# Kernel tuning notes

Measured on AMD Instinct MI355X. Metric: run time of the kernel, lower is better.

## Reference

```python
import jax, jax.numpy as jnp
import numpy as np

D_MODEL = 2048
N_HEADS = 16
D_K = D_MODEL // N_HEADS
NB_FEAT = 8  # ceil(ln(2048))
BLOCK_H = 1
BLOCK_W = 1
EPS = 1e-6


def setup_inputs() -> dict:
    key = jax.random.key(0)
    ks = jax.random.split(key, 8)
    B, S = 2, 4096
    q = jax.random.normal(ks[0], (B, S, D_MODEL), dtype=jnp.float32)
    k = jax.random.normal(ks[1], (B, S, D_MODEL), dtype=jnp.float32)
    v = jax.random.normal(ks[2], (B, S, D_MODEL), dtype=jnp.float32)
    # torch Linear weights [out, in]
    w_q = jax.random.normal(ks[3], (D_MODEL, D_MODEL), dtype=jnp.float32) / np.sqrt(D_MODEL)
    w_k = jax.random.normal(ks[4], (D_MODEL, D_MODEL), dtype=jnp.float32) / np.sqrt(D_MODEL)
    w_v = jax.random.normal(ks[5], (D_MODEL, D_MODEL), dtype=jnp.float32) / np.sqrt(D_MODEL)
    w_o = jax.random.normal(ks[6], (D_MODEL, D_MODEL), dtype=jnp.float32) / np.sqrt(D_MODEL)
    omega = jax.random.normal(ks[7], (NB_FEAT, D_K), dtype=jnp.float32) / np.sqrt(D_K)
    return {"q": q, "k": k, "v": v, "w_q": w_q, "w_k": w_k, "w_v": w_v, "w_o": w_o, "omega": omega}


def _kernel(x):
    # kernel_type == 'exp'
    return jnp.exp(-0.5 * x * x)


def reference(q, k, v, w_q, w_k, w_v, w_o, omega):
    B, Sq, D = q.shape
    Sk = k.shape[1]
    # projections (torch Linear: x @ W.T), split heads -> [B, S, H, d_k]
    qh = (q @ w_q.T).reshape(B, Sq, N_HEADS, D_K)
    kh = (k @ w_k.T).reshape(B, Sk, N_HEADS, D_K)
    vh = (v @ w_v.T).reshape(B, Sk, N_HEADS, D_K)
    # random-feature maps -> [B, S, H, nb]
    q_prime = _kernel(jnp.einsum('bshd,nd->bshn', qh, omega))
    k_prime = _kernel(jnp.einsum('bshd,nd->bshn', kh, omega))
    q_prime = q_prime / (q_prime.sum(-1, keepdims=True) + EPS)
    k_prime = k_prime / (k_prime.sum(-1, keepdims=True) + EPS)
    # causal prefix sums along sequence
    K_cum = jnp.cumsum(k_prime, axis=1)                                   # [B,S,H,nb]
    KV_cum = jnp.cumsum(k_prime[..., None] * vh[..., None, :], axis=1)    # [B,S,H,nb,d_k]
    # blockwise causal key selection
    q_idx = jnp.arange(Sq)
    key_idx = jnp.minimum((q_idx // BLOCK_H + 1) * BLOCK_W - 1, Sk - 1)   # [Sq]
    K_sel = K_cum[:, key_idx]    # [B,Sq,H,nb]
    KV_sel = KV_cum[:, key_idx]  # [B,Sq,H,nb,d_k]
    numerator = jnp.einsum('bshn,bshnd->bshd', q_prime, KV_sel)
    denominator = jnp.sum(q_prime * K_sel, axis=-1, keepdims=True)
    out = numerator / (denominator + EPS)
    out = out.reshape(B, Sq, D)
    return out @ w_o.T
```

## Files before the change

### kernel.cpp

```cpp
#include <hip/hip_runtime.h>
#include <hip/hip_bf16.h>
#include <cstdint>

#define B_SZ 2
#define S_LEN 4096
#define R_TOT 8192
#define DM 2048
#define NH 16
#define DK 128
#define NFEAT 8
#define CHUNK 128
#define NCHUNK 32
#define KSPL 512
#define EPSF 1e-6f

typedef short bf16x8_t __attribute__((ext_vector_type(8)));
typedef float f32x4_t __attribute__((ext_vector_type(4)));

__device__ __forceinline__ ushort f2bf(float f) {
  uint32_t u = __float_as_uint(f);
  u += 0x7FFF + ((u >> 16) & 1);
  return (ushort)(u >> 16);
}
__device__ __forceinline__ float bf2f(ushort u) {
  return __uint_as_float(((uint32_t)u) << 16);
}

__global__ __launch_bounds__(256) void cast_f32_bf16(const float* __restrict__ src,
                                                     ushort* __restrict__ dst, int n4) {
  int i = blockIdx.x * 256 + threadIdx.x;
  if (i >= n4) return;
  float4 f = reinterpret_cast<const float4*>(src)[i];
  ushort4 o;
  o.x = f2bf(f.x); o.y = f2bf(f.y); o.z = f2bf(f.z); o.w = f2bf(f.w);
  reinterpret_cast<ushort4*>(dst)[i] = o;
}

__global__ __launch_bounds__(256) void fold_kernel(const float* __restrict__ W,
                                                   const float* __restrict__ omega,
                                                   ushort* __restrict__ O) {
  __shared__ float som[NFEAT * DK];
  const int h = blockIdx.y;
  const int j = blockIdx.x * 256 + threadIdx.x;
  for (int i = threadIdx.x; i < NFEAT * DK; i += 256) som[i] = omega[i];
  __syncthreads();
  float acc[NFEAT] = {0.f, 0.f, 0.f, 0.f, 0.f, 0.f, 0.f, 0.f};
  for (int d = 0; d < DK; d++) {
    const float w = W[(size_t)(h * DK + d) * DM + j];
#pragma unroll
    for (int n = 0; n < NFEAT; n++) acc[n] += w * som[n * DK + d];
  }
#pragma unroll
  for (int n = 0; n < NFEAT; n++) O[(size_t)(h * NFEAT + n) * DM + j] = f2bf(acc[n]);
}

template<int BF16OUT>
__global__ __launch_bounds__(512, 1) void gemm256(const ushort* __restrict__ A,
                                                  const ushort* __restrict__ Bm,
                                                  void* __restrict__ Cv,
                                                  int M, int N, int K) {
  __shared__ ushort lds[8 * 8192];
  const int tid = threadIdx.x;
  const int wave = tid >> 6, lane = tid & 63;
  const int wm = wave >> 2, wn = wave & 3;
  const int NKT = K >> 6;

  const int nb = N >> 8;
  const int cpx = gridDim.x >> 3;
  const int swz = (blockIdx.x & 7) * cpx + (blockIdx.x >> 3);
  const int bx = swz % nb, by = swz / nb;
  const int m0 = by * 256, n0 = bx * 256;

  auto stage = [&](int bufi, int ab, int kh, int kt, const ushort* G, int r0) {
    ushort* Lr = lds + (((bufi << 1) | ab) << 1 | kh) * 8192;
#pragma unroll
    for (int j = 0; j < 2; j++) {
      const int c = j * 512 + wave * 64 + lane;
      const int row = c >> 2, slot = c & 3;
      const int ss = slot ^ ((row >> 1) & 3);
      const ushort* g = G + (size_t)(r0 + row) * K + kt * 64 + kh * 32 + ss * 8;
      __builtin_amdgcn_global_load_lds(
          (const __attribute__((address_space(1))) void*)g,
          (__attribute__((address_space(3))) void*)(Lr + (j * 512 + wave * 64) * 8), 16, 0, 0);
    }
  };
  auto rdA = [&](int bufi, int kh, int m) -> bf16x8_t {
    const int row = wm * 128 + m * 16 + (lane & 15);
    const int slot = (lane >> 4) ^ ((row >> 1) & 3);
    return *reinterpret_cast<const bf16x8_t*>(lds + ((bufi << 2) | kh) * 8192 + row * 32 + slot * 8);
  };
  auto rdB = [&](int bufi, int kh, int nf) -> bf16x8_t {
    const int row = wn * 64 + nf * 16 + (lane & 15);
    const int slot = (lane >> 4) ^ ((row >> 1) & 3);
    return *reinterpret_cast<const bf16x8_t*>(lds + (((bufi << 1) | 1) << 1 | kh) * 8192 + row * 32 + slot * 8);
  };

  f32x4_t acc[8][4];
#pragma unroll
  for (int m = 0; m < 8; m++)
#pragma unroll
    for (int nf = 0; nf < 4; nf++) acc[m][nf] = (f32x4_t){0.f, 0.f, 0.f, 0.f};

  stage(0, 0, 0, 0, A, m0);  stage(0, 1, 0, 0, Bm, n0);
  stage(0, 0, 1, 0, A, m0);  stage(0, 1, 1, 0, Bm, n0);
  stage(1, 0, 0, 1, A, m0);  stage(1, 1, 0, 1, Bm, n0);
  asm volatile("s_waitcnt vmcnt(4)" ::: "memory");
  __builtin_amdgcn_s_barrier();
  __builtin_amdgcn_sched_barrier(0);

  bf16x8_t afr[8], b0, b1;
  for (int t = 0; t < NKT; t++) {
    const int buf = t & 1;
#pragma unroll
    for (int m = 0; m < 8; m++) afr[m] = rdA(buf, 0, m);
    b0 = rdB(buf, 0, 0); b1 = rdB(buf, 0, 1);
    if (t + 1 < NKT) { stage(buf ^ 1, 0, 1, t + 1, A, m0); stage(buf ^ 1, 1, 1, t + 1, Bm, n0); }
    __builtin_amdgcn_s_barrier();
    __builtin_amdgcn_s_setprio(1);
#pragma unroll
    for (int m = 0; m < 8; m++) {
      acc[m][0] = __builtin_amdgcn_mfma_f32_16x16x32_bf16(afr[m], b0, acc[m][0], 0, 0, 0);
      acc[m][1] = __builtin_amdgcn_mfma_f32_16x16x32_bf16(afr[m], b1, acc[m][1], 0, 0, 0);
    }
    __builtin_amdgcn_s_setprio(0);
    __builtin_amdgcn_s_barrier();
    __builtin_amdgcn_sched_barrier(0);
    b0 = rdB(buf, 0, 2); b1 = rdB(buf, 0, 3);
    __builtin_amdgcn_s_barrier();
    __builtin_amdgcn_s_setprio(1);
#pragma unroll
    for (int m = 0; m < 8; m++) {
      acc[m][2] = __builtin_amdgcn_mfma_f32_16x16x32_bf16(afr[m], b0, acc[m][2], 0, 0, 0);
      acc[m][3] = __builtin_amdgcn_mfma_f32_16x16x32_bf16(afr[m], b1, acc[m][3], 0, 0, 0);
    }
    __builtin_amdgcn_s_setprio(0);
    __builtin_amdgcn_s_barrier();
    __builtin_amdgcn_sched_barrier(0);
#pragma unroll
    for (int m = 0; m < 8; m++) afr[m] = rdA(buf, 1, m);
    b0 = rdB(buf, 1, 0); b1 = rdB(buf, 1, 1);
    if (t + 2 < NKT) { stage(buf, 0, 0, t + 2, A, m0); stage(buf, 1, 0, t + 2, Bm, n0); }
    __builtin_amdgcn_s_barrier();
    __builtin_amdgcn_s_setprio(1);
#pragma unroll
    for (int m = 0; m < 8; m++) {
      acc[m][0] = __builtin_amdgcn_mfma_f32_16x16x32_bf16(afr[m], b0, acc[m][0], 0, 0, 0);
      acc[m][1] = __builtin_amdgcn_mfma_f32_16x16x32_bf16(afr[m], b1, acc[m][1], 0, 0, 0);
    }
    __builtin_amdgcn_s_setprio(0);
    __builtin_amdgcn_s_barrier();
    __builtin_amdgcn_sched_barrier(0);
    b0 = rdB(buf, 1, 2); b1 = rdB(buf, 1, 3);
    __builtin_amdgcn_s_barrier();
    __builtin_amdgcn_s_setprio(1);
#pragma unroll
    for (int m = 0; m < 8; m++) {
      acc[m][2] = __builtin_amdgcn_mfma_f32_16x16x32_bf16(afr[m], b0, acc[m][2], 0, 0, 0);
      acc[m][3] = __builtin_amdgcn_mfma_f32_16x16x32_bf16(afr[m], b1, acc[m][3], 0, 0, 0);
    }
    __builtin_amdgcn_s_setprio(0);
    if (t + 2 < NKT) { asm volatile("s_waitcnt vmcnt(4)" ::: "memory"); }
    else             { asm volatile("s_waitcnt vmcnt(0)" ::: "memory"); }
    __builtin_amdgcn_s_barrier();
    __builtin_amdgcn_sched_barrier(0);
  }

#pragma unroll
  for (int m = 0; m < 8; m++) {
    const int rb = m0 + wm * 128 + m * 16 + (lane >> 4) * 4;
#pragma unroll
    for (int nf = 0; nf < 4; nf++) {
      const int col = n0 + wn * 64 + nf * 16 + (lane & 15);
#pragma unroll
      for (int r = 0; r < 4; r++) {
        const float val = acc[m][nf][r];
        if (BF16OUT)
          ((ushort*)Cv)[(size_t)(rb + r) * N + col] = f2bf(val);
        else
          ((float*)Cv)[(size_t)(rb + r) * N + col] = val;
      }
    }
  }
}

__global__ __launch_bounds__(256) void gemm_thin(const ushort* __restrict__ A,
                                                 const ushort* __restrict__ Bm,
                                                 float* __restrict__ P,
                                                 int M, int K) {
  __shared__ ushort lds_a[128 * 32];
  __shared__ ushort lds_b[128 * 32];
  const int t = threadIdx.x;
  const int wave = t >> 6, lane = t & 63;
  const int spl = blockIdx.x;
  const int m0 = blockIdx.y * 128;
  const int kb = spl * KSPL;
  const int wm = wave >> 1, wn = wave & 1;

  f32x4_t acc[4][4];
#pragma unroll
  for (int i = 0; i < 4; i++)
#pragma unroll
    for (int j = 0; j < 4; j++) acc[i][j] = (f32x4_t){0.f, 0.f, 0.f, 0.f};

  const int srow = lane >> 2;
  const int skoff = (lane & 3) * 8;

  for (int k0 = kb; k0 < kb + KSPL; k0 += 32) {
#pragma unroll
    for (int i = 0; i < 2; i++) {
      const int rgrp = i * 4 + wave;
      const int row = rgrp * 16 + srow;
      const ushort* ga = A + (size_t)(m0 + row) * K + (k0 + skoff);
      const ushort* gb = Bm + (size_t)row * K + (k0 + skoff);
      __builtin_amdgcn_global_load_lds(
          (const __attribute__((address_space(1))) void*)ga,
          (__attribute__((address_space(3))) void*)(lds_a + rgrp * 512), 16, 0, 0);
      __builtin_amdgcn_global_load_lds(
          (const __attribute__((address_space(1))) void*)gb,
          (__attribute__((address_space(3))) void*)(lds_b + rgrp * 512), 16, 0, 0);
    }
    __syncthreads();
    bf16x8_t af[4], bfr[4];
#pragma unroll
    for (int i = 0; i < 4; i++) {
      af[i]  = *reinterpret_cast<const bf16x8_t*>(
          lds_a + (wm * 64 + i * 16 + (lane & 15)) * 32 + (lane >> 4) * 8);
      bfr[i] = *reinterpret_cast<const bf16x8_t*>(
          lds_b + (wn * 64 + i * 16 + (lane & 15)) * 32 + (lane >> 4) * 8);
    }
#pragma unroll
    for (int i = 0; i < 4; i++)
#pragma unroll
      for (int j = 0; j < 4; j++)
        acc[i][j] = __builtin_amdgcn_mfma_f32_16x16x32_bf16(af[i], bfr[j], acc[i][j], 0, 0, 0);
    __syncthreads();
  }

  float* Pp = P + (size_t)spl * ((size_t)R_TOT * 128);
#pragma unroll
  for (int i = 0; i < 4; i++) {
    const int rb = m0 + wm * 64 + i * 16 + (lane >> 4) * 4;
#pragma unroll
    for (int j = 0; j < 4; j++) {
      const int col = wn * 64 + j * 16 + (lane & 15);
#pragma unroll
      for (int r = 0; r < 4; r++)
        Pp[(size_t)(rb + r) * 128 + col] = acc[i][j][r];
    }
  }
}

__global__ __launch_bounds__(256) void feat2_kernel(const float* __restrict__ P,
                                                    float* __restrict__ F) {
  const int g = blockIdx.x * 256 + threadIdx.x;
  const int row = g >> 4, h = g & 15;
  float4 a = {0.f, 0.f, 0.f, 0.f}, c = {0.f, 0.f, 0.f, 0.f};
#pragma unroll
  for (int s = 0; s < 4; s++) {
    const float4* xp = reinterpret_cast<const float4*>(
        P + (size_t)s * ((size_t)R_TOT * 128) + (size_t)row * 128 + h * NFEAT);
    const float4 u = xp[0], w = xp[1];
    a.x += u.x; a.y += u.y; a.z += u.z; a.w += u.w;
    c.x += w.x; c.y += w.y; c.z += w.z; c.w += w.w;
  }
  float x[8] = {a.x, a.y, a.z, a.w, c.x, c.y, c.z, c.w};
  float f[8], s = 0.f;
#pragma unroll
  for (int n = 0; n < 8; n++) { f[n] = __expf(-0.5f * x[n] * x[n]); s += f[n]; }
  const float inv = 1.f / (s + EPSF);
  const int b = row >> 12, sidx = row & 4095;
  float* out = F + ((size_t)(h * 2 + b) * 4096 + sidx) * 8;
  float4 o0 = {f[0] * inv, f[1] * inv, f[2] * inv, f[3] * inv};
  float4 o1 = {f[4] * inv, f[5] * inv, f[6] * inv, f[7] * inv};
  reinterpret_cast<float4*>(out)[0] = o0;
  reinterpret_cast<float4*>(out)[1] = o1;
}

__global__ __launch_bounds__(128) void chunk_sum_kernel(const float* __restrict__ KF,
                                                        const ushort* __restrict__ VH,
                                                        float* __restrict__ CKV,
                                                        float* __restrict__ CK) {
  const int cid = blockIdx.x;
  const int c = cid & 31, bh = cid >> 5, b = bh >> 4, h = bh & 15;
  const int d = threadIdx.x;
  __shared__ float s_kf[CHUNK * 8];
  const size_t fbase = ((size_t)(h * 2 + b) * 4096 + (size_t)c * CHUNK) * 8;
  {
    float4 a0 = *reinterpret_cast<const float4*>(KF + fbase + d * 8);
    float4 a1 = *reinterpret_cast<const float4*>(KF + fbase + d * 8 + 4);
    *reinterpret_cast<float4*>(s_kf + d * 8) = a0;
    *reinterpret_cast<float4*>(s_kf + d * 8 + 4) = a1;
  }
  __syncthreads();
  float kv[8] = {0, 0, 0, 0, 0, 0, 0, 0};
  float ks = 0.f;
  const ushort* vp = VH + ((size_t)b * S_LEN + (size_t)c * CHUNK) * DM + h * DK + d;
  for (int s = 0; s < CHUNK; s++) {
    const float v = bf2f(vp[(size_t)s * DM]);
#pragma unroll
    for (int n = 0; n < 8; n++) kv[n] += s_kf[s * 8 + n] * v;
    ks += s_kf[s * 8 + (d & 7)];
  }
#pragma unroll
  for (int n = 0; n < 8; n++) CKV[((size_t)cid * 8 + n) * 128 + d] = kv[n];
  if (d < 8) CK[cid * 8 + d] = ks;
}

__global__ __launch_bounds__(128) void chunk_scan2(float* __restrict__ CKV,
                                                   float* __restrict__ CK) {
  const int bh = blockIdx.x >> 3, n = blockIdx.x & 7;
  const int d = threadIdx.x;
  float v[NCHUNK];
#pragma unroll
  for (int c = 0; c < NCHUNK; c++)
    v[c] = CKV[((size_t)(bh * NCHUNK + c) * 8 + n) * 128 + d];
  float run = 0.f;
#pragma unroll
  for (int c = 0; c < NCHUNK; c++) {
    const float tv = v[c];
    CKV[((size_t)(bh * NCHUNK + c) * 8 + n) * 128 + d] = run;
    run += tv;
  }
  if (d < 32) {
    const int i = (bh * NCHUNK + d) * 8 + n;
    const float orig = CK[i];
    float inc = orig;
#pragma unroll
    for (int off = 1; off < 32; off <<= 1) {
      const float o = __shfl_up(inc, off, 32);
      if (d >= off) inc += o;
    }
    CK[i] = inc - orig;
  }
}

__global__ __launch_bounds__(128) void attn_scan_kernel(const float* __restrict__ QF,
                                                        const float* __restrict__ KF,
                                                        const ushort* __restrict__ VH,
                                                        const float* __restrict__ CKV,
                                                        const float* __restrict__ CK,
                                                        ushort* __restrict__ AO) {
  const int cid = blockIdx.x;
  const int c = cid & 31, bh = cid >> 5, b = bh >> 4, h = bh & 15;
  const int d = threadIdx.x;
  __shared__ float s_qf[CHUNK * 8];
  __shared__ float s_kf[CHUNK * 8];
  const size_t fbase = ((size_t)(h * 2 + b) * 4096 + (size_t)c * CHUNK) * 8;
  {
    float4 a0 = *reinterpret_cast<const float4*>(QF + fbase + d * 8);
    float4 a1 = *reinterpret_cast<const float4*>(QF + fbase + d * 8 + 4);
    float4 b0 = *reinterpret_cast<const float4*>(KF + fbase + d * 8);
    float4 b1 = *reinterpret_cast<const float4*>(KF + fbase + d * 8 + 4);
    *reinterpret_cast<float4*>(s_qf + d * 8) = a0;
    *reinterpret_cast<float4*>(s_qf + d * 8 + 4) = a1;
    *reinterpret_cast<float4*>(s_kf + d * 8) = b0;
    *reinterpret_cast<float4*>(s_kf + d * 8 + 4) = b1;
  }
  float kv[8], krun[8];
#pragma unroll
  for (int n = 0; n < 8; n++) kv[n] = CKV[((size_t)cid * 8 + n) * 128 + d];
#pragma unroll
  for (int n = 0; n < 8; n++) krun[n] = CK[cid * 8 + n];
  __syncthreads();
  const size_t row0 = (size_t)b * S_LEN + (size_t)c * CHUNK;
  const ushort* vp = VH + row0 * DM + h * DK + d;
  ushort* op = AO + row0 * DM + h * DK + d;
  for (int s = 0; s < CHUNK; s++) {
    const float v = bf2f(vp[(size_t)s * DM]);
    float num = 0.f, den = 0.f;
#pragma unroll
    for (int n = 0; n < 8; n++) {
      const float kf = s_kf[s * 8 + n];
      kv[n] += kf * v;
      krun[n] += kf;
      const float qf = s_qf[s * 8 + n];
      num += qf * kv[n];
      den += qf * krun[n];
    }
    op[(size_t)s * DM] = f2bf(num / (den + EPSF));
  }
}

extern "C" void kernel_launch(void* const* d_in, const int* in_sizes, int n_in,
                              void* d_out, int out_size, void* d_ws, size_t ws_size,
                              hipStream_t stream) {
  const float* q     = (const float*)d_in[0];
  const float* k     = (const float*)d_in[1];
  const float* v     = (const float*)d_in[2];
  const float* w_q   = (const float*)d_in[3];
  const float* w_k   = (const float*)d_in[4];
  const float* w_v   = (const float*)d_in[5];
  const float* w_o   = (const float*)d_in[6];
  const float* omega = (const float*)d_in[7];

  char* ws = (char*)d_ws;
  const size_t DD2 = (size_t)DM * DM * 2;
  const size_t OD2 = (size_t)NH * NFEAT * DM * 2;
  const size_t RD2 = (size_t)R_TOT * DM * 2;
  const size_t X4  = (size_t)R_TOT * NH * NFEAT * 4;

  ushort* wvb = (ushort*)(ws);
  ushort* wob = (ushort*)(ws + DD2);
  ushort* oqb = (ushort*)(ws + 2 * DD2);
  ushort* okb = (ushort*)(ws + 2 * DD2 + OD2);
  ushort* xb  = (ushort*)(ws + 2 * DD2 + 2 * OD2);
  ushort* vhb = (ushort*)(ws + 2 * DD2 + 2 * OD2 + RD2);
  float*  xp4 = (float*) (ws + 2 * DD2 + 2 * OD2 + RD2);
  float*  qf  = (float*) (ws + 2 * DD2 + 2 * OD2 + 2 * RD2);
  float*  kf  = (float*) (ws + 2 * DD2 + 2 * OD2 + 2 * RD2 + X4);
  float*  ckv = (float*) (ws + 2 * DD2 + 2 * OD2 + 2 * RD2 + 2 * X4);
  float*  ck  = (float*) (ws + 2 * DD2 + 2 * OD2 + 2 * RD2 + 3 * X4);
  ushort* ao  = xb;

  const int n4_in = R_TOT * DM / 4;
  const int n4_w  = DM * DM / 4;

  cast_f32_bf16<<<dim3(n4_w / 256), 256, 0, stream>>>(w_v, wvb, n4_w);
  cast_f32_bf16<<<dim3(n4_w / 256), 256, 0, stream>>>(w_o, wob, n4_w);
  fold_kernel<<<dim3(DM / 256, NH), 256, 0, stream>>>(w_q, omega, oqb);
  fold_kernel<<<dim3(DM / 256, NH), 256, 0, stream>>>(w_k, omega, okb);

  dim3 gg_thin(DM / KSPL, R_TOT / 128);

  cast_f32_bf16<<<dim3(n4_in / 256), 256, 0, stream>>>(q, xb, n4_in);
  gemm_thin<<<gg_thin, 256, 0, stream>>>(xb, oqb, xp4, R_TOT, DM);
  feat2_kernel<<<dim3(R_TOT * NH / 256), 256, 0, stream>>>(xp4, qf);

  cast_f32_bf16<<<dim3(n4_in / 256), 256, 0, stream>>>(k, xb, n4_in);
  gemm_thin<<<gg_thin, 256, 0, stream>>>(xb, okb, xp4, R_TOT, DM);
  feat2_kernel<<<dim3(R_TOT * NH / 256), 256, 0, stream>>>(xp4, kf);

  cast_f32_bf16<<<dim3(n4_in / 256), 256, 0, stream>>>(v, xb, n4_in);
  gemm256<1><<<dim3((R_TOT / 256) * (DM / 256)), 512, 0, stream>>>(xb, wvb, (void*)vhb, R_TOT, DM, DM);

  chunk_sum_kernel<<<dim3(B_SZ * NH * NCHUNK), 128, 0, stream>>>(kf, vhb, ckv, ck);
  chunk_scan2<<<dim3(B_SZ * NH * 8), 128, 0, stream>>>(ckv, ck);
  attn_scan_kernel<<<dim3(B_SZ * NH * NCHUNK), 128, 0, stream>>>(qf, kf, vhb, ckv, ck, ao);

  gemm256<0><<<dim3((R_TOT / 256) * (DM / 256)), 512, 0, stream>>>(ao, wob, d_out, R_TOT, DM, DM);
}
```

Before: 349.2 us.

## Reschedule GEMM main loop into quarter-tile MFMA clusters with interleaved staging

Restructures the bf16 MFMA GEMM inner loop. Each half-k step is now split into two clusters of 16 MFMAs: four A fragments by four B fragments. The A and B global-to-LDS stages are issued separately between clusters, and explicit lgkmcnt waits are placed before each cluster. Boundary iterations now always issue loads by clamping the tile index (redundant loads at the tail) rather than branching, and vmcnt waits become a uniform count. The aim is to spread global loads more evenly and cut register pressure from holding 8 A fragments. The cost is extra redundant loads at the end and more barriers per iteration.

Measured after the change: 350.3 us. Within noise of the previous version (+0.3%).

```diff
diff --git a/kernel.cpp b/kernel.cpp
--- a/kernel.cpp
+++ b/kernel.cpp
@@ -104,66 +104,125 @@
   stage(0, 0, 0, 0, A, m0);  stage(0, 1, 0, 0, Bm, n0);
   stage(0, 0, 1, 0, A, m0);  stage(0, 1, 1, 0, Bm, n0);
   stage(1, 0, 0, 1, A, m0);  stage(1, 1, 0, 1, Bm, n0);
-  asm volatile("s_waitcnt vmcnt(4)" ::: "memory");
+  asm volatile("s_waitcnt vmcnt(8)" ::: "memory");
   __builtin_amdgcn_s_barrier();
   __builtin_amdgcn_sched_barrier(0);
 
-  bf16x8_t afr[8], b0, b1;
+  bf16x8_t a0, a1, a2, a3, b0, b1, b2, b3;
   for (int t = 0; t < NKT; t++) {
     const int buf = t & 1;
-#pragma unroll
-    for (int m = 0; m < 8; m++) afr[m] = rdA(buf, 0, m);
-    b0 = rdB(buf, 0, 0); b1 = rdB(buf, 0, 1);
-    if (t + 1 < NKT) { stage(buf ^ 1, 0, 1, t + 1, A, m0); stage(buf ^ 1, 1, 1, t + 1, Bm, n0); }
-    __builtin_amdgcn_s_barrier();
+    const int t1 = (t + 1 < NKT) ? t + 1 : NKT - 1;
+    const int t2 = (t + 2 < NKT) ? t + 2 : NKT - 1;
+
+    a0 = rdA(buf, 0, 0); a1 = rdA(buf, 0, 1); a2 = rdA(buf, 0, 2); a3 = rdA(buf, 0, 3);
+    b0 = rdB(buf, 0, 0); b1 = rdB(buf, 0, 1); b2 = rdB(buf, 0, 2); b3 = rdB(buf, 0, 3);
+    stage(buf ^ 1, 0, 1, t1, A, m0);
+    __builtin_amdgcn_s_barrier();
+    asm volatile("s_waitcnt lgkmcnt(0)" ::: "memory");
+    __builtin_amdgcn_sched_barrier(0);
     __builtin_amdgcn_s_setprio(1);
-#pragma unroll
-    for (int m = 0; m < 8; m++) {
-      acc[m][0] = __builtin_amdgcn_mfma_f32_16x16x32_bf16(afr[m], b0, acc[m][0], 0, 0, 0);
-      acc[m][1] = __builtin_amdgcn_mfma_f32_16x16x32_bf16(afr[m], b1, acc[m][1], 0, 0, 0);
-    }
+    acc[0][0] = __builtin_amdgcn_mfma_f32_16x16x32_bf16(a0, b0, acc[0][0], 0, 0, 0);
+    acc[1][0] = __builtin_amdgcn_mfma_f32_16x16x32_bf16(a1, b0, acc[1][0], 0, 0, 0);
+    acc[2][0] = __builtin_amdgcn_mfma_f32_16x16x32_bf16(a2, b0, acc[2][0], 0, 0, 0);
+    acc[3][0] = __builtin_amdgcn_mfma_f32_16x16x32_bf16(a3, b0, acc[3][0], 0, 0, 0);
+    acc[0][1] = __builtin_amdgcn_mfma_f32_16x16x32_bf16(a0, b1, acc[0][1], 0, 0, 0);
+    acc[1][1] = __builtin_amdgcn_mfma_f32_16x16x32_bf16(a1, b1, acc[1][1], 0, 0, 0);
+    acc[2][1] = __builtin_amdgcn_mfma_f32_16x16x32_bf16(a2, b1, acc[2][1], 0, 0, 0);
+    acc[3][1] = __builtin_amdgcn_mfma_f32_16x16x32_bf16(a3, b1, acc[3][1], 0, 0, 0);
+    acc[0][2] = __builtin_amdgcn_mfma_f32_16x16x32_bf16(a0, b2, acc[0][2], 0, 0, 0);
+    acc[1][2] = __builtin_amdgcn_mfma_f32_16x16x32_bf16(a1, b2, acc[1][2], 0, 0, 0);
+    acc[2][2] = __builtin_amdgcn_mfma_f32_16x16x32_bf16(a2, b2, acc[2][2], 0, 0, 0);
+    acc[3][2] = __builtin_amdgcn_mfma_f32_16x16x32_bf16(a3, b2, acc[3][2], 0, 0, 0);
+    acc[0][3] = __builtin_amdgcn_mfma_f32_16x16x32_bf16(a0, b3, acc[0][3], 0, 0, 0);
+    acc[1][3] = __builtin_amdgcn_mfma_f32_16x16x32_bf16(a1, b3, acc[1][3], 0, 0, 0);
+    acc[2][3] = __builtin_amdgcn_mfma_f32_16x16x32_bf16(a2, b3, acc[2][3], 0, 0, 0);
+    acc[3][3] = __builtin_amdgcn_mfma_f32_16x16x32_bf16(a3, b3, acc[3][3], 0, 0, 0);
     __builtin_amdgcn_s_setprio(0);
     __builtin_amdgcn_s_barrier();
     __builtin_amdgcn_sched_barrier(0);
-    b0 = rdB(buf, 0, 2); b1 = rdB(buf, 0, 3);
-    __builtin_amdgcn_s_barrier();
+
+    a0 = rdA(buf, 0, 4); a1 = rdA(buf, 0, 5); a2 = rdA(buf, 0, 6); a3 = rdA(buf, 0, 7);
+    stage(buf ^ 1, 1, 1, t1, Bm, n0);
+    __builtin_amdgcn_s_barrier();
+    asm volatile("s_waitcnt lgkmcnt(0)" ::: "memory");
+    __builtin_amdgcn_sched_barrier(0);
     __builtin_amdgcn_s_setprio(1);
-#pragma unroll
-    for (int m = 0; m < 8; m++) {
-      acc[m][2] = __builtin_amdgcn_mfma_f32_16x16x32_bf16(afr[m], b0, acc[m][2], 0, 0, 0);
-      acc[m][3] = __builtin_amdgcn_mfma_f32_16x16x32_bf16(afr[m], b1, acc[m][3], 0, 0, 0);
-    }
+    acc[4][0] = __builtin_amdgcn_mfma_f32_16x16x32_bf16(a0, b0, acc[4][0], 0, 0, 0);
+    acc[5][0] = __builtin_amdgcn_mfma_f32_16x16x32_bf16(a1, b0, acc[5][0], 0, 0, 0);
+    acc[6][0] = __builtin_amdgcn_mfma_f32_16x16x32_bf16(a2, b0, acc[6][0], 0, 0, 0);
+    acc[7][0] = __builtin_amdgcn_mfma_f32_16x16x32_bf16(a3, b0, acc[7][0], 0, 0, 0);
+    acc[4][1] = __builtin_amdgcn_mfma_f32_16x16x32_bf16(a0, b1, acc[4][1], 0, 0, 0);
+    acc[5][1] = __builtin_amdgcn_mfma_f32_16x16x32_bf16(a1, b1, acc[5][1], 0, 0, 0);
+    acc[6][1] = __builtin_amdgcn_mfma_f32_16x16x32_bf16(a2, b1, acc[6][1], 0, 0, 0);
+    acc[7][1] = __builtin_amdgcn_mfma_f32_16x16x32_bf16(a3, b1, acc[7][1], 0, 0, 0);
+    acc[4][2] = __builtin_amdgcn_mfma_f32_16x16x32_bf16(a0, b2, acc[4][2], 0, 0, 0);
+    acc[5][2] = __builtin_amdgcn_mfma_f32_16x16x32_bf16(a1, b2, acc[5][2], 0, 0, 0);
+    acc[6][2] = __builtin_amdgcn_mfma_f32_16x16x32_bf16(a2, b2, acc[6][2], 0, 0, 0);
+    acc[7][2] = __builtin_amdgcn_mfma_f32_16x16x32_bf16(a3, b2, acc[7][2], 0, 0, 0);
+    acc[4][3] = __builtin_amdgcn_mfma_f32_16x16x32_bf16(a0, b3, acc[4][3], 0, 0, 0);
+    acc[5][3] = __builtin_amdgcn_mfma_f32_16x16x32_bf16(a1, b3, acc[5][3], 0, 0, 0);
+    acc[6][3] = __builtin_amdgcn_mfma_f32_16x16x32_bf16(a2, b3, acc[6][3], 0, 0, 0);
+    acc[7][3] = __builtin_amdgcn_mfma_f32_16x16x32_bf16(a3, b3, acc[7][3], 0, 0, 0);
     __builtin_amdgcn_s_setprio(0);
-    __builtin_amdgcn_s_barrier();
-    __builtin_amdgcn_sched_barrier(0);
-#pragma unroll
-    for (int m = 0; m < 8; m++) afr[m] = rdA(buf, 1, m);
-    b0 = rdB(buf, 1, 0); b1 = rdB(buf, 1, 1);
-    if (t + 2 < NKT) { stage(buf, 0, 0, t + 2, A, m0); stage(buf, 1, 0, t + 2, Bm, n0); }
-    __builtin_amdgcn_s_barrier();
+    asm volatile("s_waitcnt vmcnt(8)" ::: "memory");
+    __builtin_amdgcn_s_barrier();
+    __builtin_amdgcn_sched_barrier(0);
+
+    a0 = rdA(buf, 1, 0); a1 = rdA(buf, 1, 1); a2 = rdA(buf, 1, 2); a3 = rdA(buf, 1, 3);
+    b0 = rdB(buf, 1, 0); b1 = rdB(buf, 1, 1); b2 = rdB(buf, 1, 2); b3 = rdB(buf, 1, 3);
+    stage(buf, 0, 0, t2, A, m0);
+    __builtin_amdgcn_s_barrier();
+    asm volatile("s_waitcnt lgkmcnt(0)" ::: "memory");
+    __builtin_amdgcn_sched_barrier(0);
     __builtin_amdgcn_s_setprio(1);
-#pragma unroll
-    for (int m = 0; m < 8; m++) {
-      acc[m][0] = __builtin_amdgcn_mfma_f32_16x16x32_bf16(afr[m], b0, acc[m][0], 0, 0, 0);
-      acc[m][1] = __builtin_amdgcn_mfma_f32_16x16x32_bf16(afr[m], b1, acc[m][1], 0, 0, 0);
-    }
+    acc[0][0] = __builtin_amdgcn_mfma_f32_16x16x32_bf16(a0, b0, acc[0][0], 0, 0, 0);
+    acc[1][0] = __builtin_amdgcn_mfma_f32_16x16x32_bf16(a1, b0, acc[1][0], 0, 0, 0);
+    acc[2][0] = __builtin_amdgcn_mfma_f32_16x16x32_bf16(a2, b0, acc[2][0], 0, 0, 0);
+    acc[3][0] = __builtin_amdgcn_mfma_f32_16x16x32_bf16(a3, b0, acc[3][0], 0, 0, 0);
+    acc[0][1] = __builtin_amdgcn_mfma_f32_16x16x32_bf16(a0, b1, acc[0][1], 0, 0, 0);
+    acc[1][1] = __builtin_amdgcn_mfma_f32_16x16x32_bf16(a1, b1, acc[1][1], 0, 0, 0);
+    acc[2][1] = __builtin_amdgcn_mfma_f32_16x16x32_bf16(a2, b1, acc[2][1], 0, 0, 0);
+    acc[3][1] = __builtin_amdgcn_mfma_f32_16x16x32_bf16(a3, b1, acc[3][1], 0, 0, 0);
+    acc[0][2] = __builtin_amdgcn_mfma_f32_16x16x32_bf16(a0, b2, acc[0][2], 0, 0, 0);
+    acc[1][2] = __builtin_amdgcn_mfma_f32_16x16x32_bf16(a1, b2, acc[1][2], 0, 0, 0);
+    acc[2][2] = __builtin_amdgcn_mfma_f32_16x16x32_bf16(a2, b2, acc[2][2], 0, 0, 0);
+    acc[3][2] = __builtin_amdgcn_mfma_f32_16x16x32_bf16(a3, b2, acc[3][2], 0, 0, 0);
+    acc[0][3] = __builtin_amdgcn_mfma_f32_16x16x32_bf16(a0, b3, acc[0][3], 0, 0, 0);
+    acc[1][3] = __builtin_amdgcn_mfma_f32_16x16x32_bf16(a1, b3, acc[1][3], 0, 0, 0);
+    acc[2][3] = __builtin_amdgcn_mfma_f32_16x16x32_bf16(a2, b3, acc[2][3], 0, 0, 0);
+    acc[3][3] = __builtin_amdgcn_mfma_f32_16x16x32_bf16(a3, b3, acc[3][3], 0, 0, 0);
     __builtin_amdgcn_s_setprio(0);
     __builtin_amdgcn_s_barrier();
     __builtin_amdgcn_sched_barrier(0);
-    b0 = rdB(buf, 1, 2); b1 = rdB(buf, 1, 3);
-    __builtin_amdgcn_s_barrier();
+
+    a0 = rdA(buf, 1, 4); a1 = rdA(buf, 1, 5); a2 = rdA(buf, 1, 6); a3 = rdA(buf, 1, 7);
+    stage(buf, 1, 0, t2, Bm, n0);
+    __builtin_amdgcn_s_barrier();
+    asm volatile("s_waitcnt lgkmcnt(0)" ::: "memory");
+    __builtin_amdgcn_sched_barrier(0);
     __builtin_amdgcn_s_setprio(1);
-#pragma unroll
-    for (int m = 0; m < 8; m++) {
-      acc[m][2] = __builtin_amdgcn_mfma_f32_16x16x32_bf16(afr[m], b0, acc[m][2], 0, 0, 0);
-      acc[m][3] = __builtin_amdgcn_mfma_f32_16x16x32_bf16(afr[m], b1, acc[m][3], 0, 0, 0);
-    }
+    acc[4][0] = __builtin_amdgcn_mfma_f32_16x16x32_bf16(a0, b0, acc[4][0], 0, 0, 0);
+    acc[5][0] = __builtin_amdgcn_mfma_f32_16x16x32_bf16(a1, b0, acc[5][0], 0, 0, 0);
+    acc[6][0] = __builtin_amdgcn_mfma_f32_16x16x32_bf16(a2, b0, acc[6][0], 0, 0, 0);
+    acc[7][0] = __builtin_amdgcn_mfma_f32_16x16x32_bf16(a3, b0, acc[7][0], 0, 0, 0);
+    acc[4][1] = __builtin_amdgcn_mfma_f32_16x16x32_bf16(a0, b1, acc[4][1], 0, 0, 0);
+    acc[5][1] = __builtin_amdgcn_mfma_f32_16x16x32_bf16(a1, b1, acc[5][1], 0, 0, 0);
+    acc[6][1] = __builtin_amdgcn_mfma_f32_16x16x32_bf16(a2, b1, acc[6][1], 0, 0, 0);
+    acc[7][1] = __builtin_amdgcn_mfma_f32_16x16x32_bf16(a3, b1, acc[7][1], 0, 0, 0);
+    acc[4][2] = __builtin_amdgcn_mfma_f32_16x16x32_bf16(a0, b2, acc[4][2], 0, 0, 0);
+    acc[5][2] = __builtin_amdgcn_mfma_f32_16x16x32_bf16(a1, b2, acc[5][2], 0, 0, 0);
+    acc[6][2] = __builtin_amdgcn_mfma_f32_16x16x32_bf16(a2, b2, acc[6][2], 0, 0, 0);
+    acc[7][2] = __builtin_amdgcn_mfma_f32_16x16x32_bf16(a3, b2, acc[7][2], 0, 0, 0);
+    acc[4][3] = __builtin_amdgcn_mfma_f32_16x16x32_bf16(a0, b3, acc[4][3], 0, 0, 0);
+    acc[5][3] = __builtin_amdgcn_mfma_f32_16x16x32_bf16(a1, b3, acc[5][3], 0, 0, 0);
+    acc[6][3] = __builtin_amdgcn_mfma_f32_16x16x32_bf16(a2, b3, acc[6][3], 0, 0, 0);
+    acc[7][3] = __builtin_amdgcn_mfma_f32_16x16x32_bf16(a3, b3, acc[7][3], 0, 0, 0);
     __builtin_amdgcn_s_setprio(0);
-    if (t + 2 < NKT) { asm volatile("s_waitcnt vmcnt(4)" ::: "memory"); }
-    else             { asm volatile("s_waitcnt vmcnt(0)" ::: "memory"); }
-    __builtin_amdgcn_s_barrier();
-    __builtin_amdgcn_sched_barrier(0);
-  }
+    asm volatile("s_waitcnt vmcnt(8)" ::: "memory");
+    __builtin_amdgcn_s_barrier();
+    __builtin_amdgcn_sched_barrier(0);
+  }
+  asm volatile("s_waitcnt vmcnt(0)" ::: "memory");
 
 #pragma unroll
   for (int m = 0; m < 8; m++) {
```

## Software-pipeline LDS fragment reads with MFMA blocks in gemm256 main loop

Applied to the files above, without the earlier changes.

Restructures the GEMM inner loop so that LDS fragment reads for the next quarter-tile are issued while MFMAs on the current fragments run, using double-buffered A/B register sets and four 16-MFMA blocks per iteration. Global-to-LDS staging is split into finer per-operand pieces and spread across the phases, with adjusted vmcnt waits. Tail iterations now re-stage clamped tiles instead of skipping, which adds redundant loads to reduce branching. It raises register pressure and depends on the vmcnt counts being correct for LDS buffer safety.

Result: no change. 343.9 us (-1.5%).

```diff
diff --git a/kernel.cpp b/kernel.cpp
--- a/kernel.cpp
+++ b/kernel.cpp
@@ -54,6 +54,24 @@
   for (int n = 0; n < NFEAT; n++) O[(size_t)(h * NFEAT + n) * DM + j] = f2bf(acc[n]);
 }
 
+#define MFMA_BLK(mb, A0_, A1_, A2_, A3_, B0_, B1_, B2_, B3_)                                  \
+  acc[mb + 0][0] = __builtin_amdgcn_mfma_f32_16x16x32_bf16(A0_, B0_, acc[mb + 0][0], 0, 0, 0); \
+  acc[mb + 1][0] = __builtin_amdgcn_mfma_f32_16x16x32_bf16(A1_, B0_, acc[mb + 1][0], 0, 0, 0); \
+  acc[mb + 2][0] = __builtin_amdgcn_mfma_f32_16x16x32_bf16(A2_, B0_, acc[mb + 2][0], 0, 0, 0); \
+  acc[mb + 3][0] = __builtin_amdgcn_mfma_f32_16x16x32_bf16(A3_, B0_, acc[mb + 3][0], 0, 0, 0); \
+  acc[mb + 0][1] = __builtin_amdgcn_mfma_f32_16x16x32_bf16(A0_, B1_, acc[mb + 0][1], 0, 0, 0); \
+  acc[mb + 1][1] = __builtin_amdgcn_mfma_f32_16x16x32_bf16(A1_, B1_, acc[mb + 1][1], 0, 0, 0); \
+  acc[mb + 2][1] = __builtin_amdgcn_mfma_f32_16x16x32_bf16(A2_, B1_, acc[mb + 2][1], 0, 0, 0); \
+  acc[mb + 3][1] = __builtin_amdgcn_mfma_f32_16x16x32_bf16(A3_, B1_, acc[mb + 3][1], 0, 0, 0); \
+  acc[mb + 0][2] = __builtin_amdgcn_mfma_f32_16x16x32_bf16(A0_, B2_, acc[mb + 0][2], 0, 0, 0); \
+  acc[mb + 1][2] = __builtin_amdgcn_mfma_f32_16x16x32_bf16(A1_, B2_, acc[mb + 1][2], 0, 0, 0); \
+  acc[mb + 2][2] = __builtin_amdgcn_mfma_f32_16x16x32_bf16(A2_, B2_, acc[mb + 2][2], 0, 0, 0); \
+  acc[mb + 3][2] = __builtin_amdgcn_mfma_f32_16x16x32_bf16(A3_, B2_, acc[mb + 3][2], 0, 0, 0); \
+  acc[mb + 0][3] = __builtin_amdgcn_mfma_f32_16x16x32_bf16(A0_, B3_, acc[mb + 0][3], 0, 0, 0); \
+  acc[mb + 1][3] = __builtin_amdgcn_mfma_f32_16x16x32_bf16(A1_, B3_, acc[mb + 1][3], 0, 0, 0); \
+  acc[mb + 2][3] = __builtin_amdgcn_mfma_f32_16x16x32_bf16(A2_, B3_, acc[mb + 2][3], 0, 0, 0); \
+  acc[mb + 3][3] = __builtin_amdgcn_mfma_f32_16x16x32_bf16(A3_, B3_, acc[mb + 3][3], 0, 0, 0);
+
 template<int BF16OUT>
 __global__ __launch_bounds__(512, 1) void gemm256(const ushort* __restrict__ A,
                                                   const ushort* __restrict__ Bm,
@@ -104,66 +122,56 @@
   stage(0, 0, 0, 0, A, m0);  stage(0, 1, 0, 0, Bm, n0);
   stage(0, 0, 1, 0, A, m0);  stage(0, 1, 1, 0, Bm, n0);
   stage(1, 0, 0, 1, A, m0);  stage(1, 1, 0, 1, Bm, n0);
-  asm volatile("s_waitcnt vmcnt(4)" ::: "memory");
+  asm volatile("s_waitcnt vmcnt(8)" ::: "memory");
   __builtin_amdgcn_s_barrier();
   __builtin_amdgcn_sched_barrier(0);
 
-  bf16x8_t afr[8], b0, b1;
+  bf16x8_t pA0 = rdA(0, 0, 0), pA1 = rdA(0, 0, 1), pA2 = rdA(0, 0, 2), pA3 = rdA(0, 0, 3);
+  bf16x8_t B00 = rdB(0, 0, 0), B01 = rdB(0, 0, 1), B02 = rdB(0, 0, 2), B03 = rdB(0, 0, 3);
+  bf16x8_t qA0, qA1, qA2, qA3, B10, B11, B12, B13;
+
   for (int t = 0; t < NKT; t++) {
     const int buf = t & 1;
-#pragma unroll
-    for (int m = 0; m < 8; m++) afr[m] = rdA(buf, 0, m);
-    b0 = rdB(buf, 0, 0); b1 = rdB(buf, 0, 1);
-    if (t + 1 < NKT) { stage(buf ^ 1, 0, 1, t + 1, A, m0); stage(buf ^ 1, 1, 1, t + 1, Bm, n0); }
+    const int t1 = (t + 1 < NKT) ? t + 1 : NKT - 1;
+    const int t2 = (t + 2 < NKT) ? t + 2 : NKT - 1;
+
+    qA0 = rdA(buf, 0, 4); qA1 = rdA(buf, 0, 5); qA2 = rdA(buf, 0, 6); qA3 = rdA(buf, 0, 7);
+    stage(buf ^ 1, 0, 1, t1, A, m0);
+    __builtin_amdgcn_s_setprio(1);
+    MFMA_BLK(0, pA0, pA1, pA2, pA3, B00, B01, B02, B03)
+    __builtin_amdgcn_s_setprio(0);
+    asm volatile("s_waitcnt vmcnt(6)" ::: "memory");
     __builtin_amdgcn_s_barrier();
+    __builtin_amdgcn_sched_barrier(0);
+
+    pA0 = rdA(buf, 1, 0); pA1 = rdA(buf, 1, 1); pA2 = rdA(buf, 1, 2); pA3 = rdA(buf, 1, 3);
+    B10 = rdB(buf, 1, 0); B11 = rdB(buf, 1, 1); B12 = rdB(buf, 1, 2); B13 = rdB(buf, 1, 3);
+    stage(buf ^ 1, 1, 1, t1, Bm, n0);
     __builtin_amdgcn_s_setprio(1);
-#pragma unroll
-    for (int m = 0; m < 8; m++) {
-      acc[m][0] = __builtin_amdgcn_mfma_f32_16x16x32_bf16(afr[m], b0, acc[m][0], 0, 0, 0);
-      acc[m][1] = __builtin_amdgcn_mfma_f32_16x16x32_bf16(afr[m], b1, acc[m][1], 0, 0, 0);
-    }
+    MFMA_BLK(4, qA0, qA1, qA2, qA3, B00, B01, B02, B03)
     __builtin_amdgcn_s_setprio(0);
     __builtin_amdgcn_s_barrier();
     __builtin_amdgcn_sched_barrier(0);
-    b0 = rdB(buf, 0, 2); b1 = rdB(buf, 0, 3);
+
+    qA0 = rdA(buf, 1, 4); qA1 = rdA(buf, 1, 5); qA2 = rdA(buf, 1, 6); qA3 = rdA(buf, 1, 7);
+    stage(buf, 0, 0, t2, A, m0);
+    __builtin_amdgcn_s_setprio(1);
+    MFMA_BLK(0, pA0, pA1, pA2, pA3, B10, B11, B12, B13)
+    __builtin_amdgcn_s_setprio(0);
+    asm volatile("s_waitcnt vmcnt(6)" ::: "memory");
     __builtin_amdgcn_s_barrier();
+    __builtin_amdgcn_sched_barrier(0);
+
+    pA0 = rdA(buf ^ 1, 0, 0); pA1 = rdA(buf ^ 1, 0, 1); pA2 = rdA(buf ^ 1, 0, 2); pA3 = rdA(buf ^ 1, 0, 3);
+    B00 = rdB(buf ^ 1, 0, 0); B01 = rdB(buf ^ 1, 0, 1); B02 = rdB(buf ^ 1, 0, 2); B03 = rdB(buf ^ 1, 0, 3);
+    stage(buf, 1, 0, t2, Bm, n0);
     __builtin_amdgcn_s_setprio(1);
-#pragma unroll
-    for (int m = 0; m < 8; m++) {
-      acc[m][2] = __builtin_amdgcn_mfma_f32_16x16x32_bf16(afr[m], b0, acc[m][2], 0, 0, 0);
-      acc[m][3] = __builtin_amdgcn_mfma_f32_16x16x32_bf16(afr[m], b1, acc[m][3], 0, 0, 0);
-    }
+    MFMA_BLK(4, qA0, qA1, qA2, qA3, B10, B11, B12, B13)
     __builtin_amdgcn_s_setprio(0);
     __builtin_amdgcn_s_barrier();
     __builtin_amdgcn_sched_barrier(0);
-#pragma unroll
-    for (int m = 0; m < 8; m++) afr[m] = rdA(buf, 1, m);
-    b0 = rdB(buf, 1, 0); b1 = rdB(buf, 1, 1);
-    if (t + 2 < NKT) { stage(buf, 0, 0, t + 2, A, m0); stage(buf, 1, 0, t + 2, Bm, n0); }
-    __builtin_amdgcn_s_barrier();
-    __builtin_amdgcn_s_setprio(1);
-#pragma unroll
-    for (int m = 0; m < 8; m++) {
-      acc[m][0] = __builtin_amdgcn_mfma_f32_16x16x32_bf16(afr[m], b0, acc[m][0], 0, 0, 0);
-      acc[m][1] = __builtin_amdgcn_mfma_f32_16x16x32_bf16(afr[m], b1, acc[m][1], 0, 0, 0);
-    }
-    __builtin_amdgcn_s_setprio(0);
-    __builtin_amdgcn_s_barrier();
-    __builtin_amdgcn_sched_barrier(0);
-    b0 = rdB(buf, 1, 2); b1 = rdB(buf, 1, 3);
-    __builtin_amdgcn_s_barrier();
-    __builtin_amdgcn_s_setprio(1);
-#pragma unroll
-    for (int m = 0; m < 8; m++) {
-      acc[m][2] = __builtin_amdgcn_mfma_f32_16x16x32_bf16(afr[m], b0, acc[m][2], 0, 0, 0);
-      acc[m][3] = __builtin_amdgcn_mfma_f32_16x16x32_bf16(afr[m], b1, acc[m][3], 0, 0, 0);
-    }
-    __builtin_amdgcn_s_setprio(0);
-    if (t + 2 < NKT) { asm volatile("s_waitcnt vmcnt(4)" ::: "memory"); }
-    else             { asm volatile("s_waitcnt vmcnt(0)" ::: "memory"); }
-    __builtin_amdgcn_s_barrier();
-    __builtin_amdgcn_sched_barrier(0);
-  }
+  }
+  asm volatile("s_waitcnt vmcnt(0)" ::: "memory");
 
 #pragma unroll
   for (int m = 0; m < 8; m++) {
```
